# Kernel optimization log

Hardware: AMD Instinct MI355X
Metric: run time of the kernel (lower is better)

Reference implementation:

```python
import jax, jax.numpy as jnp
import numpy as np

# ---- static config ----
G = 4          # num graphs
NG = 512       # nodes per graph
N = G * NG     # total nodes
E = 32768      # num edges
IN_DIM = 128
HID = 32
HEADS = 4
HC = HID * HEADS  # 128
OUT_DIM = 32
N_LAYERS = 2
GRID = 500
Q = 20
NEG_SLOPE = 0.2
QUANTILES = jnp.asarray(np.linspace(0.0, 1.0, Q), jnp.float32)  # [Q]


def setup_inputs() -> dict:
    key = jax.random.key(0)
    ks = jax.random.split(key, 32)
    inp = {}
    inp['x'] = jax.random.normal(ks[0], (N, IN_DIM), jnp.float32)
    inp['edge_index'] = jax.random.randint(ks[1], (2, E), 0, N).astype(jnp.int64)
    inp['batch'] = (jnp.arange(N) // NG).astype(jnp.int64)
    # GATConv params (2 layers, both 128 -> 4 heads x 32, concat)
    for l, (kin,) in enumerate([(IN_DIM,), (HC,)]):
        s = 1.0 / np.sqrt(kin)
        inp[f'W{l}'] = jax.random.normal(ks[2 + 4 * l], (kin, HC), jnp.float32) * s
        inp[f'as{l}'] = jax.random.normal(ks[3 + 4 * l], (HEADS, HID), jnp.float32) * s
        inp[f'ad{l}'] = jax.random.normal(ks[4 + 4 * l], (HEADS, HID), jnp.float32) * s
        inp[f'b{l}'] = jnp.zeros((HC,), jnp.float32)
    for l in range(N_LAYERS + 1):
        inp[f'lpW{l}'] = jax.random.normal(ks[10 + 2 * l], (HC, OUT_DIM), jnp.float32) * (1.0 / np.sqrt(HC))
        inp[f'lpb{l}'] = jnp.zeros((OUT_DIM,), jnp.float32)
    for l in range(N_LAYERS + 1):
        inp[f'kW{l}'] = jax.random.normal(ks[16 + 2 * l], (HC * Q, OUT_DIM), jnp.float32) * (1.0 / np.sqrt(HC * Q))
        inp[f'kb{l}'] = jnp.zeros((OUT_DIM,), jnp.float32)
    inp['pool_w'] = jnp.ones((2,), jnp.float32) / 2.0
    inp['beta'] = jax.random.normal(ks[22], (OUT_DIM,), jnp.float32)
    inp['h0'] = jax.random.normal(ks[23], (1,), jnp.float32)
    return inp


def _gat_layer(x, src, dst, W, a_src, a_dst, bias):
    # PyG GATConv (concat=True, add_self_loops=True, negative_slope=0.2), eval mode
    n = x.shape[0]
    xh = (x @ W).reshape(n, HEADS, HID)              # [N,H,C]
    loop = jnp.arange(n)
    s = jnp.concatenate([src, loop])                 # [E+N]
    d = jnp.concatenate([dst, loop])
    al_s = jnp.einsum('nhc,hc->nh', xh, a_src)       # [N,H]
    al_d = jnp.einsum('nhc,hc->nh', xh, a_dst)
    e = jax.nn.leaky_relu(al_s[s] + al_d[d], NEG_SLOPE)   # [E+N,H]
    e_max = jax.ops.segment_max(e, d, num_segments=n)     # stable softmax per dst
    e = jnp.exp(e - e_max[d])
    denom = jax.ops.segment_sum(e, d, num_segments=n)
    alpha = e / (denom[d] + 1e-16)                   # [E+N,H]
    out = jax.ops.segment_sum(alpha[:, :, None] * xh[s], d, num_segments=n)
    return out.reshape(n, HC) + bias


def _kde_per_graph(xg):
    # xg: [Ng, D] -> [D*Q] soft-quantile features via grid KDE
    n = xg.shape[0]
    mn = xg.min(axis=0) - 1e-6                       # [D]
    mx = xg.max(axis=0) + 1e-6
    grid = jnp.linspace(0.0, 1.0, GRID)[:, None] * (mx - mn) + mn   # [Gp,D]
    std = xg.std(axis=0) + 1e-8 / 3
    h = 1.06 * std * float(n) ** (-0.2)              # [D]
    u = (grid[:, None, :] - xg[None, :, :]) / h      # [Gp,Ng,D]  (dominant tensor)
    kern = jnp.exp(-0.5 * u * u) / (h * np.sqrt(2.0 * np.pi))
    density = kern.mean(axis=1)                      # [Gp,D]
    cdf = jnp.cumsum(density, axis=0)
    cdf = cdf / jnp.clip(cdf[-1:], 1e-8)
    dist = jnp.abs(cdf[:, :, None] - QUANTILES)      # [Gp,D,Q]
    w = jax.nn.sigmoid(-100.0 * dist)
    w = w / (w.sum(axis=0, keepdims=True) + 1e-8)
    qv = (grid[:, :, None] * w).sum(axis=0)          # [D,Q]
    return qv.reshape(-1)


def _readout(cur, lpW, lpb, kW, kb, pool_w):
    xr = cur.reshape(G, NG, -1)
    pooled = jnp.stack([xr.mean(axis=1), xr.max(axis=1)], axis=0)   # [2,G,D]
    wp = (pooled * pool_w[:, None, None]).sum(axis=0)               # [G,D]
    h = wp @ lpW + lpb                                              # [G,out]
    kf = jax.vmap(_kde_per_graph)(xr)                               # [G,D*Q]
    return h, kf @ kW + kb


def reference(x, edge_index, batch, W0, as0, ad0, b0, W1, as1, ad1, b1,
              lpW0, lpb0, lpW1, lpb1, lpW2, lpb2,
              kW0, kb0, kW1, kb1, kW2, kb2, pool_w, beta, h0):
    src, dst = edge_index[0], edge_index[1]
    convs = [(W0, as0, ad0, b0), (W1, as1, ad1, b1)]
    lps = [(lpW0, lpb0), (lpW1, lpb1), (lpW2, lpb2)]
    kps = [(kW0, kb0), (kW1, kb1), (kW2, kb2)]
    cur = x
    h_list, kde_list = [], []
    for i in range(N_LAYERS):
        h, kp = _readout(cur, lps[i][0], lps[i][1], kps[i][0], kps[i][1], pool_w)
        h_list.append(h); kde_list.append(kp)
        cur = _gat_layer(cur, src, dst, *convs[i])
        if i != N_LAYERS - 1:
            cur = jax.nn.relu(cur)
    h, kp = _readout(cur, lps[-1][0], lps[-1][1], kps[-1][0], kps[-1][1], pool_w)
    h_list.append(h); kde_list.append(kp)
    main_out = jnp.stack(h_list).mean(axis=0)        # [G,out]
    kde_out = jnp.stack(kde_list).mean(axis=0)
    risk = (main_out + kde_out) @ beta + h0          # [G]
    return risk
```

## Files before the change

### kernel.cpp

```cpp
#include <hip/hip_runtime.h>
#include <math.h>

#define GNUM 4
#define NG 512
#define NN 2048
#define EE 32768
#define HC 128
#define HEADS 4
#define HID 32
#define GRID_PTS 500
#define QN 20
#define ODIM 32
#define MAXE 160

#define LOG2E 1.44269504088896340736f
#define NEG_HALF_LOG2E -0.72134752044448170368f
#define N_POW_M02 0.2871745887492588f
#define SIG_K 144.269504089f

__device__ __forceinline__ float fexp2(float x){ return __builtin_amdgcn_exp2f(x); }
__device__ __forceinline__ float frcp(float x){ return __builtin_amdgcn_rcpf(x); }

struct SmemKDE {
  __align__(16) float2 xs[NG];
  float4 wred4[8];
  float sc[4];
  float wsum[8], woff[9];
  float redw[QN][8], redg[QN][8];
  float qs[QN];
};
struct SmemXW  { float rows[4][HC]; };
struct SmemGat {
  int   ssrc[4][MAXE];
  float sexp[4][MAXE][HEADS];
  float smax[4][HEADS], sfac[4][HEADS];
};
union Smem { SmemKDE kde; SmemXW xw; SmemGat gat; };

__device__ void kde_phase(Smem& sm, const float* __restrict__ cur, int do_relu, int trans,
        const float* __restrict__ kW, const float* __restrict__ kb, float* __restrict__ kacc,
        const float* __restrict__ lpW, const float* __restrict__ lpb,
        const float* __restrict__ poolw, float* __restrict__ macc){
  int b = blockIdx.x;
  int g = b >> 7, d = b & 127;
  int t = threadIdx.x;
  int lane = t & 63, wave = t >> 6;
  float v = trans ? cur[(size_t)d*NN + g*NG + t]
                  : cur[((size_t)g*NG + t)*HC + d];
  if (do_relu) v = fmaxf(v, 0.f);
  sm.kde.xs[t] = make_float2(v, v*v);
  float mn=v, mx=v, smv=v, sq=v*v;
  #pragma unroll
  for (int m=32; m>0; m>>=1){
    mn = fminf(mn, __shfl_xor(mn, m, 64));
    mx = fmaxf(mx, __shfl_xor(mx, m, 64));
    smv += __shfl_xor(smv, m, 64);
    sq += __shfl_xor(sq, m, 64);
  }
  if (lane==0) sm.kde.wred4[wave] = make_float4(mn,mx,smv,sq);
  __syncthreads();
  if (t==0){
    float4 r = sm.kde.wred4[0];
    #pragma unroll
    for (int i=1;i<8;++i){
      float4 bb = sm.kde.wred4[i];
      r.x = fminf(r.x,bb.x); r.y = fmaxf(r.y,bb.y); r.z += bb.z; r.w += bb.w;
    }
    float mean = r.z * (1.f/NG);
    float var  = fmaxf(r.w*(1.f/NG) - mean*mean, 0.f);
    float sd   = sqrtf(var) + (1e-8f/3.f);
    float h    = 1.06f * sd * N_POW_M02;
    float lo = r.x - 1e-6f, hi = r.y + 1e-6f;
    sm.kde.sc[0] = lo;
    sm.kde.sc[1] = (hi-lo)*(1.f/(GRID_PTS-1));
    sm.kde.sc[2] = NEG_HALF_LOG2E/(h*h);
    sm.kde.sc[3] = poolw[0]*mean + poolw[1]*r.y;
  }
  __syncthreads();
  float lo = sm.kde.sc[0], st = sm.kde.sc[1], kk = sm.kde.sc[2];
  float gv = lo + st*(float)t;
  float acc = 0.f;
  if (t < GRID_PTS){
    float c0 = kk*gv*gv, c1 = -2.f*kk*gv;
    const float4* p4 = (const float4*)sm.kde.xs;
    #pragma unroll 4
    for (int i=0;i<NG/2;++i){
      float4 s2 = p4[i];
      acc += fexp2(fmaf(kk, s2.y, fmaf(c1, s2.x, c0)));
      acc += fexp2(fmaf(kk, s2.w, fmaf(c1, s2.z, c0)));
    }
  }
  float sv = acc;
  #pragma unroll
  for (int off=1; off<64; off<<=1){
    float n = __shfl_up(sv, off, 64);
    if (lane >= off) sv += n;
  }
  if (lane==63) sm.kde.wsum[wave] = sv;
  __syncthreads();
  if (t==0){
    float r2 = 0.f;
    #pragma unroll
    for (int i=0;i<8;++i){ sm.kde.woff[i]=r2; r2+=sm.kde.wsum[i]; }
    sm.kde.woff[8]=r2;
  }
  if (t < QN*8){ ((float*)sm.kde.redw)[t]=0.f; ((float*)sm.kde.redg)[t]=0.f; }
  __syncthreads();
  float invt = 1.f/fmaxf(sm.kde.woff[8], 1e-8f);
  float c = (sv + sm.kde.woff[wave]) * invt;
  float cw0 = __shfl(c, 0, 64), cw1 = __shfl(c, 63, 64);
  int qlo = max(0, (int)ceilf((cw0 - 0.17f)*(float)(QN-1)));
  int qhi = min(QN-1, (int)floorf((cw1 + 0.17f)*(float)(QN-1)));
  for (int q=qlo; q<=qhi; ++q){
    float w = 0.f;
    if (t < GRID_PTS){
      float dist = fabsf(c - (float)q*(1.f/(QN-1)));
      w = frcp(1.f + fexp2(SIG_K*dist));
    }
    float gw = gv*w;
    #pragma unroll
    for (int m=32;m>0;m>>=1){
      w  += __shfl_xor(w,  m, 64);
      gw += __shfl_xor(gw, m, 64);
    }
    if (lane==0){ sm.kde.redw[q][wave]=w; sm.kde.redg[q][wave]=gw; }
  }
  __syncthreads();
  if (t < QN){
    float sw=0.f, sgw=0.f;
    #pragma unroll
    for (int i=0;i<8;++i){ sw+=sm.kde.redw[t][i]; sgw+=sm.kde.redg[t][i]; }
    sm.kde.qs[t] = sgw / (sw + 1e-8f);
  }
  __syncthreads();
  if (t < ODIM){
    int shard = (d >> 5) & 3;
    float a = 0.f;
    const float* kwb = kW + (size_t)d*QN*ODIM + t;
    #pragma unroll
    for (int q=0;q<QN;++q) a += sm.kde.qs[q]*kwb[q*ODIM];
    if (d==0) a += kb[t];
    atomicAdd(&kacc[shard*128 + g*ODIM + t], a);
    float bb = sm.kde.sc[3]*lpW[d*ODIM + t];
    if (d==0) bb += lpb[t];
    atomicAdd(&macc[shard*128 + g*ODIM + t], bb);
  }
  __syncthreads();
}

__device__ float gather_core(Smem& sm, int d, int sub, int tl,
        const int* __restrict__ csr, const int* __restrict__ pos,
        const float* __restrict__ als, const float* __restrict__ ald,
        const float* __restrict__ xh, const float* __restrict__ bias){
  int deg = min(pos[d], MAXE-1);
  int E = deg + 1;
  const int* base = csr + d*MAXE;
  float a0 = ald[d*4+0], a1 = ald[d*4+1], a2 = ald[d*4+2], a3 = ald[d*4+3];
  for (int i=tl; i<E; i+=128){
    int s = (i < deg) ? base[i] : d;
    sm.gat.ssrc[sub][i] = s;
    float e0 = als[s*4+0]+a0, e1 = als[s*4+1]+a1, e2 = als[s*4+2]+a2, e3 = als[s*4+3]+a3;
    e0 = (e0>=0.f)? e0 : 0.2f*e0;
    e1 = (e1>=0.f)? e1 : 0.2f*e1;
    e2 = (e2>=0.f)? e2 : 0.2f*e2;
    e3 = (e3>=0.f)? e3 : 0.2f*e3;
    sm.gat.sexp[sub][i][0]=e0; sm.gat.sexp[sub][i][1]=e1;
    sm.gat.sexp[sub][i][2]=e2; sm.gat.sexp[sub][i][3]=e3;
  }
  __syncthreads();
  if (tl < HEADS){
    float m = -INFINITY;
    for (int i=0;i<E;++i) m = fmaxf(m, sm.gat.sexp[sub][i][tl]);
    sm.gat.smax[sub][tl] = m;
  }
  __syncthreads();
  for (int i=tl; i<E; i+=128){
    #pragma unroll
    for (int h=0;h<HEADS;++h)
      sm.gat.sexp[sub][i][h] = fexp2(LOG2E*(sm.gat.sexp[sub][i][h]-sm.gat.smax[sub][h]));
  }
  __syncthreads();
  if (tl < HEADS){
    float sdn = 0.f;
    for (int i=0;i<E;++i) sdn += sm.gat.sexp[sub][i][tl];
    sm.gat.sfac[sub][tl] = 1.f/(sdn + 1e-16f);
  }
  __syncthreads();
  int h = tl >> 5;
  float fac = sm.gat.sfac[sub][h];
  float acc = bias[tl];
  for (int i=0;i<E;++i)
    acc += sm.gat.sexp[sub][i][h]*fac * xh[(size_t)sm.gat.ssrc[sub][i]*HC + tl];
  __syncthreads();
  return acc;
}

__device__ void xw_emit(Smem& sm, int sub, int j, int n,
        const float* __restrict__ W, const float* __restrict__ as_, const float* __restrict__ ad_,
        float* __restrict__ xh, float* __restrict__ als, float* __restrict__ ald){
  float acc = 0.f;
  #pragma unroll 8
  for (int c2=0;c2<HC;++c2)
    acc += sm.xw.rows[sub][c2]*W[(size_t)c2*HC + j];
  xh[(size_t)n*HC + j] = acc;
  int h = j >> 5, cc = j & 31;
  float ps = acc*as_[h*HID+cc], pd = acc*ad_[h*HID+cc];
  #pragma unroll
  for (int m=16;m>0;m>>=1){
    ps += __shfl_xor(ps, m, 32);
    pd += __shfl_xor(pd, m, 32);
  }
  if (cc==0){ als[n*HEADS+h]=ps; ald[n*HEADS+h]=pd; }
}

__device__ void write_transposed(Smem& sm, int t, int n0, float* __restrict__ curT){
  if (t < HC){
    float4 v = make_float4(sm.xw.rows[0][t], sm.xw.rows[1][t],
                           sm.xw.rows[2][t], sm.xw.rows[3][t]);
    *(float4*)(curT + (size_t)t*NN + n0) = v;
  }
}

__global__ __launch_bounds__(1024) void k_zero(int* __restrict__ pos, float* __restrict__ acc){
  int t = threadIdx.x;
  pos[t] = 0; pos[t+1024] = 0;
  acc[t] = 0.f; acc[t+1024] = 0.f;
  if (t < 1024) acc[t+2048] = 0.f;
}

__global__ __launch_bounds__(512) void k_L0(const float* __restrict__ x,
        const float* __restrict__ kW, const float* __restrict__ kb, float* __restrict__ kacc,
        const float* __restrict__ lpW, const float* __restrict__ lpb,
        const float* __restrict__ poolw, float* __restrict__ macc,
        const float* __restrict__ W, const float* __restrict__ as_, const float* __restrict__ ad_,
        float* __restrict__ xh, float* __restrict__ als, float* __restrict__ ald,
        const int* __restrict__ src, const int* __restrict__ dst,
        int* __restrict__ pos, int* __restrict__ csr){
  __shared__ Smem sm;
  int t = threadIdx.x;
  if (blockIdx.x < 512){
    kde_phase(sm, x, 0, 0, kW, kb, kacc, lpW, lpb, poolw, macc);
  } else {
    int b2 = blockIdx.x - 512;
    if (t < 64){
      int e = b2*64 + t;
      int dd = dst[e];
      int pp = atomicAdd(&pos[dd], 1);
      if (pp < MAXE) csr[dd*MAXE + pp] = src[e];
    }
    int sub = t >> 7, j = t & 127;
    int n = b2*4 + sub;
    sm.xw.rows[sub][j] = x[(size_t)n*HC + j];
    __syncthreads();
    xw_emit(sm, sub, j, n, W, as_, ad_, xh, als, ald);
  }
}

__global__ __launch_bounds__(512) void k_G0(const int* __restrict__ csr, const int* __restrict__ pos,
        const float* __restrict__ als_in, const float* __restrict__ ald_in,
        const float* __restrict__ xh_in, const float* __restrict__ bias,
        float* __restrict__ cur1T,
        const float* __restrict__ W1, const float* __restrict__ as1, const float* __restrict__ ad1,
        float* __restrict__ xh2, float* __restrict__ als2, float* __restrict__ ald2){
  __shared__ Smem sm;
  int t = threadIdx.x;
  int sub = t >> 7, tl = t & 127;
  int d = blockIdx.x*4 + sub;
  float acc = gather_core(sm, d, sub, tl, csr, pos, als_in, ald_in, xh_in, bias);
  sm.xw.rows[sub][tl] = fmaxf(acc, 0.f);
  __syncthreads();
  write_transposed(sm, t, blockIdx.x*4, cur1T);
  xw_emit(sm, sub, tl, d, W1, as1, ad1, xh2, als2, ald2);
}

__global__ __launch_bounds__(512) void k_L1(const float* __restrict__ cur1T,
        const float* __restrict__ kW, const float* __restrict__ kb, float* __restrict__ kacc,
        const float* __restrict__ lpW, const float* __restrict__ lpb,
        const float* __restrict__ poolw, float* __restrict__ macc,
        const int* __restrict__ csr, const int* __restrict__ pos,
        const float* __restrict__ als2, const float* __restrict__ ald2,
        const float* __restrict__ xh2, const float* __restrict__ bias,
        float* __restrict__ cur2T){
  __shared__ Smem sm;
  int t = threadIdx.x;
  if (blockIdx.x < 512){
    kde_phase(sm, cur1T, 0, 1, kW, kb, kacc, lpW, lpb, poolw, macc);
  } else {
    int b2 = blockIdx.x - 512;
    int sub = t >> 7, tl = t & 127;
    int d = b2*4 + sub;
    float acc = gather_core(sm, d, sub, tl, csr, pos, als2, ald2, xh2, bias);
    sm.xw.rows[sub][tl] = acc;
    __syncthreads();
    write_transposed(sm, t, b2*4, cur2T);
  }
}

__global__ __launch_bounds__(512) void k_L2(const float* __restrict__ cur2T,
        const float* __restrict__ kW, const float* __restrict__ kb, float* __restrict__ kacc,
        const float* __restrict__ lpW, const float* __restrict__ lpb,
        const float* __restrict__ poolw, float* __restrict__ macc){
  __shared__ Smem sm;
  kde_phase(sm, cur2T, 0, 1, kW, kb, kacc, lpW, lpb, poolw, macc);
}

__global__ void k_final(const float* __restrict__ maccS, const float* __restrict__ kaccS,
                        const float* __restrict__ beta, const float* __restrict__ h0,
                        float* __restrict__ out){
  int t = threadIdx.x;
  int g = t >> 5, o = t & 31;
  __shared__ float sdm[128];
  float s3 = 0.f;
  #pragma unroll
  for (int l=0;l<3;++l)
    #pragma unroll
    for (int s=0;s<4;++s)
      s3 += maccS[l*512 + s*128 + t] + kaccS[l*512 + s*128 + t];
  sdm[t] = s3 * (1.f/3.f) * beta[o];
  __syncthreads();
  if ((t & 31) == 0){
    float s = 0.f;
    #pragma unroll
    for (int i=0;i<32;++i) s += sdm[g*32+i];
    out[g] = s + h0[0];
  }
}

extern "C" void kernel_launch(void* const* d_in, const int* in_sizes, int n_in,
                              void* d_out, int out_size, void* d_ws, size_t ws_size,
                              hipStream_t stream) {
  (void)in_sizes; (void)n_in; (void)out_size; (void)ws_size;
  const float* x    = (const float*)d_in[0];
  const int*   ei   = (const int*)d_in[1];
  const int*   srcp = ei;
  const int*   dstp = ei + EE;
  const float* W[2]   = {(const float*)d_in[3], (const float*)d_in[7]};
  const float* As[2]  = {(const float*)d_in[4], (const float*)d_in[8]};
  const float* Ad[2]  = {(const float*)d_in[5], (const float*)d_in[9]};
  const float* Bi[2]  = {(const float*)d_in[6], (const float*)d_in[10]};
  const float* lpW[3] = {(const float*)d_in[11], (const float*)d_in[13], (const float*)d_in[15]};
  const float* lpb[3] = {(const float*)d_in[12], (const float*)d_in[14], (const float*)d_in[16]};
  const float* kW[3]  = {(const float*)d_in[17], (const float*)d_in[19], (const float*)d_in[21]};
  const float* kb[3]  = {(const float*)d_in[18], (const float*)d_in[20], (const float*)d_in[22]};
  const float* poolw  = (const float*)d_in[23];
  const float* beta   = (const float*)d_in[24];
  const float* h0     = (const float*)d_in[25];
  float* out = (float*)d_out;

  float* ws = (float*)d_ws;
  float* cur1T = ws;
  float* cur2T = cur1T + 262144;
  float* xh    = cur2T + 262144;
  float* xh2   = xh + 262144;
  float* als   = xh2 + 262144;
  float* ald   = als + 8192;
  float* als2  = ald + 8192;
  float* ald2  = als2 + 8192;
  float* maccS = ald2 + 8192;
  float* kaccS = maccS + 1536;
  int*   pos   = (int*)(kaccS + 1536);
  int*   csr   = pos + 2048;

  k_zero<<<1, 1024, 0, stream>>>(pos, maccS);
  k_L0<<<1024, 512, 0, stream>>>(x, kW[0], kb[0], kaccS, lpW[0], lpb[0], poolw, maccS,
                                 W[0], As[0], Ad[0], xh, als, ald,
                                 srcp, dstp, pos, csr);
  k_G0<<<512, 512, 0, stream>>>(csr, pos, als, ald, xh, Bi[0], cur1T,
                                W[1], As[1], Ad[1], xh2, als2, ald2);
  k_L1<<<1024, 512, 0, stream>>>(cur1T, kW[1], kb[1], kaccS+512, lpW[1], lpb[1], poolw, maccS+512,
                                 csr, pos, als2, ald2, xh2, Bi[1], cur2T);
  k_L2<<<512, 512, 0, stream>>>(cur2T, kW[2], kb[2], kaccS+1024, lpW[2], lpb[2], poolw, maccS+1024);
  k_final<<<1, 128, 0, stream>>>(maccS, kaccS, beta, h0, out);
}
```

Measured before the change: 204.4 us.

## Remove zeroing kernel, atomics, and serial softmax reductions across GAT/KDE pipeline

Drops the zeroing kernel. Each KDE block now writes its per-dimension partials to its own slot, and k_final reduces them instead of using global atomics. CSR construction moves into per-block shared-memory counters, with each xw block scanning all edges for its own 4 destinations. The GAT softmax max and sum now use wave shuffles instead of single-thread serial loops with extra barriers. The transposed activations are stored interleaved as (v, v²) pairs, so the KDE loop reads them straight from global memory without staging in LDS. Each xw block now scans all 32K edges, which adds redundant edge reads, and the CSR slot order is no longer deterministic.

```diff
diff --git a/kernel.cpp b/kernel.cpp
--- a/kernel.cpp
+++ b/kernel.cpp
@@ -29,11 +29,10 @@
   float redw[QN][8], redg[QN][8];
   float qs[QN];
 };
-struct SmemXW  { float rows[4][HC]; };
+struct SmemXW  { float rows[4][HC]; int cnt[4]; };
 struct SmemGat {
   int   ssrc[4][MAXE];
   float sexp[4][MAXE][HEADS];
-  float smax[4][HEADS], sfac[4][HEADS];
 };
 union Smem { SmemKDE kde; SmemXW xw; SmemGat gat; };
 
@@ -45,11 +44,17 @@
   int g = b >> 7, d = b & 127;
   int t = threadIdx.x;
   int lane = t & 63, wave = t >> 6;
-  float v = trans ? cur[(size_t)d*NN + g*NG + t]
-                  : cur[((size_t)g*NG + t)*HC + d];
-  if (do_relu) v = fmaxf(v, 0.f);
-  sm.kde.xs[t] = make_float2(v, v*v);
-  float mn=v, mx=v, smv=v, sq=v*v;
+  float v, v2;
+  if (trans){
+    float2 vv = ((const float2*)cur)[(size_t)d*NN + g*NG + t];
+    v = vv.x; v2 = vv.y;
+  } else {
+    v = cur[((size_t)g*NG + t)*HC + d];
+    v2 = v*v;
+  }
+  if (do_relu){ v = fmaxf(v, 0.f); v2 = v*v; }
+  if (!trans) sm.kde.xs[t] = make_float2(v, v2);
+  float mn=v, mx=v, smv=v, sq=v2;
   #pragma unroll
   for (int m=32; m>0; m>>=1){
     mn = fminf(mn, __shfl_xor(mn, m, 64));
@@ -82,7 +87,8 @@
   float acc = 0.f;
   if (t < GRID_PTS){
     float c0 = kk*gv*gv, c1 = -2.f*kk*gv;
-    const float4* p4 = (const float4*)sm.kde.xs;
+    const float4* p4 = trans ? ((const float4*)cur) + (((size_t)d*NN + g*NG) >> 1)
+                             : (const float4*)sm.kde.xs;
     #pragma unroll 4
     for (int i=0;i<NG/2;++i){
       float4 s2 = p4[i];
@@ -134,30 +140,29 @@
   }
   __syncthreads();
   if (t < ODIM){
-    int shard = (d >> 5) & 3;
     float a = 0.f;
     const float* kwb = kW + (size_t)d*QN*ODIM + t;
     #pragma unroll
     for (int q=0;q<QN;++q) a += sm.kde.qs[q]*kwb[q*ODIM];
     if (d==0) a += kb[t];
-    atomicAdd(&kacc[shard*128 + g*ODIM + t], a);
+    kacc[(size_t)d*128 + g*ODIM + t] = a;
     float bb = sm.kde.sc[3]*lpW[d*ODIM + t];
     if (d==0) bb += lpb[t];
-    atomicAdd(&macc[shard*128 + g*ODIM + t], bb);
+    macc[(size_t)d*128 + g*ODIM + t] = bb;
   }
   __syncthreads();
 }
 
 __device__ float gather_core(Smem& sm, int d, int sub, int tl,
-        const int* __restrict__ csr, const int* __restrict__ pos,
+        const int* __restrict__ csr, const int* __restrict__ deg,
         const float* __restrict__ als, const float* __restrict__ ald,
         const float* __restrict__ xh, const float* __restrict__ bias){
-  int deg = min(pos[d], MAXE-1);
-  int E = deg + 1;
+  int dg = deg[d];
+  int E = dg + 1;
   const int* base = csr + d*MAXE;
   float a0 = ald[d*4+0], a1 = ald[d*4+1], a2 = ald[d*4+2], a3 = ald[d*4+3];
   for (int i=tl; i<E; i+=128){
-    int s = (i < deg) ? base[i] : d;
+    int s = (i < dg) ? base[i] : d;
     sm.gat.ssrc[sub][i] = s;
     float e0 = als[s*4+0]+a0, e1 = als[s*4+1]+a1, e2 = als[s*4+2]+a2, e3 = als[s*4+3]+a3;
     e0 = (e0>=0.f)? e0 : 0.2f*e0;
@@ -168,26 +173,20 @@
     sm.gat.sexp[sub][i][2]=e2; sm.gat.sexp[sub][i][3]=e3;
   }
   __syncthreads();
-  if (tl < HEADS){
-    float m = -INFINITY;
-    for (int i=0;i<E;++i) m = fmaxf(m, sm.gat.sexp[sub][i][tl]);
-    sm.gat.smax[sub][tl] = m;
-  }
-  __syncthreads();
-  for (int i=tl; i<E; i+=128){
-    #pragma unroll
-    for (int h=0;h<HEADS;++h)
-      sm.gat.sexp[sub][i][h] = fexp2(LOG2E*(sm.gat.sexp[sub][i][h]-sm.gat.smax[sub][h]));
-  }
-  __syncthreads();
-  if (tl < HEADS){
-    float sdn = 0.f;
-    for (int i=0;i<E;++i) sdn += sm.gat.sexp[sub][i][tl];
-    sm.gat.sfac[sub][tl] = 1.f/(sdn + 1e-16f);
-  }
-  __syncthreads();
-  int h = tl >> 5;
-  float fac = sm.gat.sfac[sub][h];
+  int h = tl >> 5, l32 = tl & 31;
+  float mx = -INFINITY;
+  for (int i=l32; i<E; i+=32) mx = fmaxf(mx, sm.gat.sexp[sub][i][h]);
+  #pragma unroll
+  for (int m=16; m>0; m>>=1) mx = fmaxf(mx, __shfl_xor(mx, m, 32));
+  float sdn = 0.f;
+  for (int i=l32; i<E; i+=32){
+    float ev = fexp2(LOG2E*(sm.gat.sexp[sub][i][h] - mx));
+    sm.gat.sexp[sub][i][h] = ev;
+    sdn += ev;
+  }
+  #pragma unroll
+  for (int m=16; m>0; m>>=1) sdn += __shfl_xor(sdn, m, 32);
+  float fac = 1.f/(sdn + 1e-16f);
   float acc = bias[tl];
   for (int i=0;i<E;++i)
     acc += sm.gat.sexp[sub][i][h]*fac * xh[(size_t)sm.gat.ssrc[sub][i]*HC + tl];
@@ -215,17 +214,12 @@
 
 __device__ void write_transposed(Smem& sm, int t, int n0, float* __restrict__ curT){
   if (t < HC){
-    float4 v = make_float4(sm.xw.rows[0][t], sm.xw.rows[1][t],
-                           sm.xw.rows[2][t], sm.xw.rows[3][t]);
-    *(float4*)(curT + (size_t)t*NN + n0) = v;
-  }
-}
-
-__global__ __launch_bounds__(1024) void k_zero(int* __restrict__ pos, float* __restrict__ acc){
-  int t = threadIdx.x;
-  pos[t] = 0; pos[t+1024] = 0;
-  acc[t] = 0.f; acc[t+1024] = 0.f;
-  if (t < 1024) acc[t+2048] = 0.f;
+    float v0 = sm.xw.rows[0][t], v1 = sm.xw.rows[1][t];
+    float v2 = sm.xw.rows[2][t], v3 = sm.xw.rows[3][t];
+    float4* p = (float4*)(curT + (((size_t)t*NN + n0) << 1));
+    p[0] = make_float4(v0, v0*v0, v1, v1*v1);
+    p[1] = make_float4(v2, v2*v2, v3, v3*v3);
+  }
 }
 
 __global__ __launch_bounds__(512) void k_L0(const float* __restrict__ x,
@@ -235,28 +229,34 @@
         const float* __restrict__ W, const float* __restrict__ as_, const float* __restrict__ ad_,
         float* __restrict__ xh, float* __restrict__ als, float* __restrict__ ald,
         const int* __restrict__ src, const int* __restrict__ dst,
-        int* __restrict__ pos, int* __restrict__ csr){
+        int* __restrict__ deg, int* __restrict__ csr){
   __shared__ Smem sm;
   int t = threadIdx.x;
   if (blockIdx.x < 512){
     kde_phase(sm, x, 0, 0, kW, kb, kacc, lpW, lpb, poolw, macc);
   } else {
     int b2 = blockIdx.x - 512;
-    if (t < 64){
-      int e = b2*64 + t;
-      int dd = dst[e];
-      int pp = atomicAdd(&pos[dd], 1);
-      if (pp < MAXE) csr[dd*MAXE + pp] = src[e];
-    }
     int sub = t >> 7, j = t & 127;
     int n = b2*4 + sub;
+    if (t < 4) sm.xw.cnt[t] = 0;
     sm.xw.rows[sub][j] = x[(size_t)n*HC + j];
     __syncthreads();
+    int base4 = b2*4;
+    for (int e = t; e < EE; e += 512){
+      int dd = dst[e];
+      unsigned r = (unsigned)(dd - base4);
+      if (r < 4u){
+        int p = atomicAdd(&sm.xw.cnt[r], 1);
+        if (p < MAXE) csr[dd*MAXE + p] = src[e];
+      }
+    }
     xw_emit(sm, sub, j, n, W, as_, ad_, xh, als, ald);
-  }
-}
-
-__global__ __launch_bounds__(512) void k_G0(const int* __restrict__ csr, const int* __restrict__ pos,
+    __syncthreads();
+    if (t < 4) deg[base4 + t] = min(sm.xw.cnt[t], MAXE-1);
+  }
+}
+
+__global__ __launch_bounds__(512) void k_G0(const int* __restrict__ csr, const int* __restrict__ deg,
         const float* __restrict__ als_in, const float* __restrict__ ald_in,
         const float* __restrict__ xh_in, const float* __restrict__ bias,
         float* __restrict__ cur1T,
@@ -266,7 +266,7 @@
   int t = threadIdx.x;
   int sub = t >> 7, tl = t & 127;
   int d = blockIdx.x*4 + sub;
-  float acc = gather_core(sm, d, sub, tl, csr, pos, als_in, ald_in, xh_in, bias);
+  float acc = gather_core(sm, d, sub, tl, csr, deg, als_in, ald_in, xh_in, bias);
   sm.xw.rows[sub][tl] = fmaxf(acc, 0.f);
   __syncthreads();
   write_transposed(sm, t, blockIdx.x*4, cur1T);
@@ -277,7 +277,7 @@
         const float* __restrict__ kW, const float* __restrict__ kb, float* __restrict__ kacc,
         const float* __restrict__ lpW, const float* __restrict__ lpb,
         const float* __restrict__ poolw, float* __restrict__ macc,
-        const int* __restrict__ csr, const int* __restrict__ pos,
+        const int* __restrict__ csr, const int* __restrict__ deg,
         const float* __restrict__ als2, const float* __restrict__ ald2,
         const float* __restrict__ xh2, const float* __restrict__ bias,
         float* __restrict__ cur2T){
@@ -289,7 +289,7 @@
     int b2 = blockIdx.x - 512;
     int sub = t >> 7, tl = t & 127;
     int d = b2*4 + sub;
-    float acc = gather_core(sm, d, sub, tl, csr, pos, als2, ald2, xh2, bias);
+    float acc = gather_core(sm, d, sub, tl, csr, deg, als2, ald2, xh2, bias);
     sm.xw.rows[sub][tl] = acc;
     __syncthreads();
     write_transposed(sm, t, b2*4, cur2T);
@@ -304,25 +304,25 @@
   kde_phase(sm, cur2T, 0, 1, kW, kb, kacc, lpW, lpb, poolw, macc);
 }
 
-__global__ void k_final(const float* __restrict__ maccS, const float* __restrict__ kaccS,
+__global__ __launch_bounds__(384) void k_final(const float* __restrict__ mpart, const float* __restrict__ kpart,
                         const float* __restrict__ beta, const float* __restrict__ h0,
                         float* __restrict__ out){
   int t = threadIdx.x;
-  int g = t >> 5, o = t & 31;
-  __shared__ float sdm[128];
-  float s3 = 0.f;
-  #pragma unroll
-  for (int l=0;l<3;++l)
-    #pragma unroll
-    for (int s=0;s<4;++s)
-      s3 += maccS[l*512 + s*128 + t] + kaccS[l*512 + s*128 + t];
-  sdm[t] = s3 * (1.f/3.f) * beta[o];
-  __syncthreads();
-  if ((t & 31) == 0){
-    float s = 0.f;
-    #pragma unroll
-    for (int i=0;i<32;++i) s += sdm[g*32+i];
-    out[g] = s + h0[0];
+  __shared__ float sdm[384];
+  int l = t >> 7, tt = t & 127;
+  const float* mrow = mpart + (size_t)l*16384 + tt;
+  const float* krow = kpart + (size_t)l*16384 + tt;
+  float s = 0.f;
+  #pragma unroll 8
+  for (int d2=0; d2<128; ++d2) s += mrow[(size_t)d2*128] + krow[(size_t)d2*128];
+  sdm[t] = s;
+  __syncthreads();
+  if (t < 128){
+    int g = t >> 5, o = t & 31;
+    float s3 = (sdm[t] + sdm[t+128] + sdm[t+256]) * (1.f/3.f) * beta[o];
+    #pragma unroll
+    for (int m=16; m>0; m>>=1) s3 += __shfl_xor(s3, m, 32);
+    if (o == 0) out[g] = s3 + h0[0];
   }
 }
 
@@ -349,26 +349,25 @@
 
   float* ws = (float*)d_ws;
   float* cur1T = ws;
-  float* cur2T = cur1T + 262144;
-  float* xh    = cur2T + 262144;
+  float* cur2T = cur1T + 524288;
+  float* xh    = cur2T + 524288;
   float* xh2   = xh + 262144;
   float* als   = xh2 + 262144;
   float* ald   = als + 8192;
   float* als2  = ald + 8192;
   float* ald2  = als2 + 8192;
-  float* maccS = ald2 + 8192;
-  float* kaccS = maccS + 1536;
-  int*   pos   = (int*)(kaccS + 1536);
-  int*   csr   = pos + 2048;
-
-  k_zero<<<1, 1024, 0, stream>>>(pos, maccS);
-  k_L0<<<1024, 512, 0, stream>>>(x, kW[0], kb[0], kaccS, lpW[0], lpb[0], poolw, maccS,
+  float* mpart = ald2 + 8192;
+  float* kpart = mpart + 49152;
+  int*   deg   = (int*)(kpart + 49152);
+  int*   csr   = deg + 2048;
+
+  k_L0<<<1024, 512, 0, stream>>>(x, kW[0], kb[0], kpart, lpW[0], lpb[0], poolw, mpart,
                                  W[0], As[0], Ad[0], xh, als, ald,
-                                 srcp, dstp, pos, csr);
-  k_G0<<<512, 512, 0, stream>>>(csr, pos, als, ald, xh, Bi[0], cur1T,
+                                 srcp, dstp, deg, csr);
+  k_G0<<<512, 512, 0, stream>>>(csr, deg, als, ald, xh, Bi[0], cur1T,
                                 W[1], As[1], Ad[1], xh2, als2, ald2);
-  k_L1<<<1024, 512, 0, stream>>>(cur1T, kW[1], kb[1], kaccS+512, lpW[1], lpb[1], poolw, maccS+512,
-                                 csr, pos, als2, ald2, xh2, Bi[1], cur2T);
-  k_L2<<<512, 512, 0, stream>>>(cur2T, kW[2], kb[2], kaccS+1024, lpW[2], lpb[2], poolw, maccS+1024);
-  k_final<<<1, 128, 0, stream>>>(maccS, kaccS, beta, h0, out);
-}
+  k_L1<<<1024, 512, 0, stream>>>(cur1T, kW[1], kb[1], kpart+16384, lpW[1], lpb[1], poolw, mpart+16384,
+                                 csr, deg, als2, ald2, xh2, Bi[1], cur2T);
+  k_L2<<<512, 512, 0, stream>>>(cur2T, kW[2], kb[2], kpart+32768, lpW[2], lpb[2], poolw, mpart+32768);
+  k_final<<<1, 384, 0, stream>>>(mpart, kpart, beta, h0, out);
+}
```

Result: slower. 208.6 us (+2.1%).
